# Kernel tuning notes

Measured on AMD Instinct MI355X. Metric: run time of the kernel, lower is better.

## Reference

```python
import jax, jax.numpy as jnp
import numpy as np

N = 100000      # nodes
E = 1600000     # edges (before self-loops)
DIM = 128       # input feature dim
H = 5           # attention heads
C = 10          # per-head output channels
G = 256         # graphs in batch
NEG_SLOPE = 0.2 # PyG GATConv default


def setup_inputs() -> dict:
    key = jax.random.key(0)
    ks = jax.random.split(key, 8)
    x = jax.random.normal(ks[0], (N, DIM), jnp.float32)
    edge_index = jax.random.randint(ks[1], (2, E), 0, N, dtype=jnp.int64)
    batch = jnp.sort(jax.random.randint(ks[2], (N,), 0, G, dtype=jnp.int64))
    W = jax.random.normal(ks[3], (DIM, H * C), jnp.float32) * 0.05
    att_src = jax.random.normal(ks[4], (H, C), jnp.float32) * 0.1
    att_dst = jax.random.normal(ks[5], (H, C), jnp.float32) * 0.1
    bias = jnp.zeros((H * C,), jnp.float32)
    lin_w = jax.random.normal(ks[6], (H * C, 1), jnp.float32) * 0.1
    lin_b = jnp.zeros((1,), jnp.float32)
    return {"x": x, "W": W, "att_src": att_src, "att_dst": att_dst,
            "bias": bias, "lin_w": lin_w, "lin_b": lin_b,
            "edge_index": edge_index, "batch": batch}


def reference(x, W, att_src, att_dst, bias, lin_w, lin_b, edge_index, batch):
    n = x.shape[0]
    # PyG GATConv adds self-loops by default
    loop = jnp.arange(n, dtype=edge_index.dtype)
    src = jnp.concatenate([edge_index[0], loop])  # message sources j
    dst = jnp.concatenate([edge_index[1], loop])  # message targets i

    xw = (x @ W).reshape(n, H, C)                       # [N,H,C]
    a_src = jnp.einsum('nhc,hc->nh', xw, att_src)       # [N,H]
    a_dst = jnp.einsum('nhc,hc->nh', xw, att_dst)       # [N,H]

    logits = jax.nn.leaky_relu(a_src[src] + a_dst[dst], NEG_SLOPE)  # [Etot,H]
    # segment softmax over incoming edges per target node
    m = jax.ops.segment_max(logits, dst, num_segments=n)
    ex = jnp.exp(logits - m[dst])
    denom = jax.ops.segment_sum(ex, dst, num_segments=n)
    alpha = ex / denom[dst]                              # [Etot,H]

    msg = alpha[:, :, None] * xw[src]                    # [Etot,H,C]
    out = jax.ops.segment_sum(msg, dst, num_segments=n).reshape(n, H * C) + bias
    out = jax.nn.elu(out)                                # [N,H*C]

    # global_mean_pool over graph ids
    gsum = jax.ops.segment_sum(out, batch, num_segments=G)
    cnt = jax.ops.segment_sum(jnp.ones((n,), out.dtype), batch, num_segments=G)
    h = gsum / jnp.maximum(cnt, 1.0)[:, None]            # [G,H*C]

    # dropout p=0.5 is identity at inference (training=False)
    y = jax.nn.sigmoid(h @ lin_w + lin_b)                # [G,1]
    return (h, y)
```

## Files before the change

### kernel.cpp

```cpp
#include <hip/hip_runtime.h>
#include <hip/hip_bf16.h>
#include <hip/hip_fp8.h>
#include <math.h>

#define DIM 128
#define H 5
#define C 10
#define HC 50
#define NG 256
#define NEG_SLOPE 0.2f
#define UNR 16
#define WP 136
#define LOG2E 1.4426950408889634f

#define BSH 6
#define NB 1563
#define SB_CAP 1344
#define B1_BLOCKS 391
#define B1_CHUNK 4096

#define BKN2 32
#define ROWS_LDS2 (BKN2 * 64)

typedef short short8 __attribute__((ext_vector_type(8)));
typedef float floatx4 __attribute__((ext_vector_type(4)));
typedef float floatx2 __attribute__((ext_vector_type(2)));

__device__ inline short f2bf(float f) {
  __hip_bfloat16 h = __float2bfloat16(f);
  return *reinterpret_cast<short*>(&h);
}
#if __has_builtin(__builtin_amdgcn_cvt_f32_fp8)
__device__ inline float fp8tof(int b) { return __builtin_amdgcn_cvt_f32_fp8(b, 0); }
#else
__device__ inline float fp8tof(int b) {
  __hip_fp8_e4m3 v;
  v.__x = (__hip_fp8_storage_t)b;
  return (float)v;
}
#endif
#if __has_builtin(__builtin_amdgcn_cvt_pk_f32_fp8)
__device__ inline floatx2 fp8pk2(int us) {
  return __builtin_amdgcn_cvt_pk_f32_fp8(us, false);
}
#else
__device__ inline floatx2 fp8pk2(int us) {
  floatx2 r;
  r.x = fp8tof(us & 0xff);
  r.y = fp8tof((us >> 8) & 0xff);
  return r;
}
#endif
#if __has_builtin(__builtin_amdgcn_exp2f)
__device__ inline float fexp2(float x) { return __builtin_amdgcn_exp2f(x); }
#else
__device__ inline float fexp2(float x) { return exp2f(x); }
#endif
__device__ inline unsigned char ftofp8(float f) {
  __hip_fp8_e4m3 v(f);
  return v.__x;
}

__global__ __launch_bounds__(256) void k_prep(
    const float* __restrict__ W, const float* __restrict__ att_src,
    const float* __restrict__ att_dst, short* __restrict__ swt_g,
    int* __restrict__ gcur, unsigned char* __restrict__ recb, int n) {
  int t = threadIdx.x;
  for (int i = t; i < NB; i += 256) gcur[i] = 0;
  if (t < 64) recb[((size_t)n << 6) + t] = (t < HC) ? 0x00 : 0xFE;
  for (int idx = t; idx < HC * 128; idx += 256) {
    int j = idx >> 7, k = idx & 127;
    swt_g[idx] = f2bf(W[k * HC + j]);
  }
  if (t < 128) {
    float sv[H] = {0.f, 0.f, 0.f, 0.f, 0.f};
    float dv[H] = {0.f, 0.f, 0.f, 0.f, 0.f};
#pragma unroll
    for (int c = 0; c < HC; ++c) {
      float w = W[t * HC + c];
      sv[c / C] += w * att_src[c];
      dv[c / C] += w * att_dst[c];
    }
#pragma unroll
    for (int h = 0; h < H; ++h) {
      swt_g[(HC + h) * 128 + t] = f2bf(sv[h] * LOG2E);
      swt_g[(55 + h) * 128 + t] = f2bf(dv[h] * LOG2E);
    }
  } else {
    int k = t - 128;
    for (int j = 60; j < 64; ++j) swt_g[j * 128 + k] = 0;
  }
}

__global__ __launch_bounds__(256) void k_split(
    const int* __restrict__ src, const int* __restrict__ dst,
    int* __restrict__ gcur, int* __restrict__ seg, int E_) {
  __shared__ int hist[NB], curs[NB], baser[NB];
  int tid = threadIdx.x;
  for (int i = tid; i < NB; i += 256) hist[i] = 0;
  __syncthreads();
  int e0 = blockIdx.x * B1_CHUNK;
  for (int k = 0; k < B1_CHUNK; k += 256) {
    int e = e0 + k + tid;
    if (e < E_) atomicAdd(&hist[((unsigned)dst[e]) >> BSH], 1);
  }
  __syncthreads();
  for (int i = tid; i < NB; i += 256) {
    baser[i] = hist[i] ? atomicAdd(&gcur[i], hist[i]) : 0;
    curs[i] = 0;
  }
  __syncthreads();
  for (int k = 0; k < B1_CHUNK; k += 256) {
    int e = e0 + k + tid;
    if (e < E_) {
      int d = dst[e];
      int s = ((unsigned)d) >> BSH;
      int pos = baser[s] + atomicAdd(&curs[s], 1);
      if (pos < SB_CAP) seg[(size_t)s * SB_CAP + pos] = (src[e] << 6) | (d & 63);
    }
  }
}

__global__ __launch_bounds__(256) void k_mfma(
    const float* __restrict__ x, const short* __restrict__ swt_g,
    unsigned char* __restrict__ recb, __hip_bfloat16* __restrict__ adst, int n) {
  __shared__ short swt[64 * WP];
  for (int idx = threadIdx.x; idx < 1024; idx += 256) {
    int row = idx >> 4;
    *(short8*)&swt[row * WP + (idx & 15) * 8] = *(const short8*)(swt_g + idx * 8);
  }
  __syncthreads();
  int wv = threadIdx.x >> 6, lane = threadIdx.x & 63;
  int tiles = (n + 15) >> 4;
  int tile = blockIdx.x * 4 + wv;
  if (tile >= tiles) return;
  int r = lane & 15, q = lane >> 4;
  int row = tile * 16 + r;
  const float* xr = x + (size_t)min(row, n - 1) * DIM + q * 8;
  floatx4 acc[4];
#pragma unroll
  for (int nt = 0; nt < 4; ++nt) acc[nt] = (floatx4){0.f, 0.f, 0.f, 0.f};
#pragma unroll
  for (int ks = 0; ks < 4; ++ks) {
    float4 a0 = *(const float4*)(xr + ks * 32);
    float4 a1 = *(const float4*)(xr + ks * 32 + 4);
    short8 af;
    af[0] = f2bf(a0.x); af[1] = f2bf(a0.y); af[2] = f2bf(a0.z); af[3] = f2bf(a0.w);
    af[4] = f2bf(a1.x); af[5] = f2bf(a1.y); af[6] = f2bf(a1.z); af[7] = f2bf(a1.w);
    const short* wb = &swt[r * WP + q * 8 + ks * 32];
    short8 b0 = *(const short8*)(wb);
    short8 b1 = *(const short8*)(wb + 16 * WP);
    short8 b2 = *(const short8*)(wb + 32 * WP);
    short8 b3 = *(const short8*)(wb + 48 * WP);
    acc[0] = __builtin_amdgcn_mfma_f32_16x16x32_bf16(af, b0, acc[0], 0, 0, 0);
    acc[1] = __builtin_amdgcn_mfma_f32_16x16x32_bf16(af, b1, acc[1], 0, 0, 0);
    acc[2] = __builtin_amdgcn_mfma_f32_16x16x32_bf16(af, b2, acc[2], 0, 0, 0);
    acc[3] = __builtin_amdgcn_mfma_f32_16x16x32_bf16(af, b3, acc[3], 0, 0, 0);
  }
#pragma unroll
  for (int reg = 0; reg < 4; ++reg) {
    int nrow = tile * 16 + q * 4 + reg;
    if (nrow >= n) continue;
    size_t base = (size_t)nrow << 6;
#pragma unroll
    for (int nt = 0; nt < 4; ++nt) {
      int col = nt * 16 + r;
      float v = acc[nt][reg];
      if (col < 50) {
        recb[base + col] = ftofp8(v);
      } else if (col < 55) {
        unsigned char bv = ftofp8(v);
        *(unsigned short*)(recb + base + 50 + 2 * (col - 50)) =
            (unsigned short)(bv | (bv << 8));
      } else if (col < 60) {
        adst[(size_t)nrow * H + (col - 55)] = __float2bfloat16(v);
      }
    }
  }
}

__global__ __launch_bounds__(256) void k_bin_gat(
    const int* __restrict__ seg, const int* __restrict__ gcur,
    const unsigned char* __restrict__ recb, const __hip_bfloat16* __restrict__ adst,
    const float* __restrict__ bias, float* __restrict__ out_node, int n) {
  __shared__ int rows[ROWS_LDS2];
  int tid = threadIdx.x;
  int blk = blockIdx.x;
  int b = blk >> 1;
  int half32 = blk & 1;
  int lo = (b << BSH) + (half32 << 5);
  int hi = min(lo + BKN2, n);
  for (int k = tid; k < ROWS_LDS2; k += 256) rows[k] = n;
  __syncthreads();
  int cnt = min(gcur[b], SB_CAP);
  for (int k = tid; k < cnt; k += 256) {
    int e = seg[(size_t)b * SB_CAP + k];
    int dl = e & 63;
    if ((dl >> 5) == half32) {
      int s = ((unsigned)e) >> 6;
      int base = (dl & 31) << 6;
      int off = s & 63;
      int old = atomicExch(&rows[base + off], s);
      int probes = 0;
      while (old != n && probes < 128) {
        off = (off + 1) & 63;
        old = atomicExch(&rows[base + off], old);
        ++probes;
      }
    }
  }
  __syncthreads();

  int w = tid >> 6, lane = tid & 63;
  int nn = hi - lo;
  int pairsN = (nn + 1) >> 1;
  int hl = lane & 31;
  int hf = lane >> 5;
  bool chl = hl < 25;
  int h = hl / 5;
  int bpidx = ((hf << 5) + 25 + h) << 2;
  unsigned rowoff = (unsigned)(hl << 1);

  for (int pr = w; pr < pairsN; pr += 4) {
    int i0l = pr * 2;
    int i1l = min(i0l + 1, nn - 1);
    int i0 = lo + i0l, i1 = lo + i1l;
    int iown = hf ? i1 : i0;
    float adi = 0.f;
    if (chl) adi = __bfloat162float(adst[(size_t)iown * H + h]);

    int jraw0 = rows[(i0l << 6) | lane];
    int jraw1 = rows[(i1l << 6) | lane];
    bool v0 = (unsigned)jraw0 < (unsigned)n;
    unsigned long long mk0 = __ballot(v0);
    int deg0 = __popcll(mk0);
    int bel0 = __popcll(mk0 & ((1ull << lane) - 1ull));
    int jc0 = __builtin_amdgcn_ds_permute((v0 ? bel0 : (deg0 + lane - bel0)) << 2,
                                          v0 ? jraw0 : n);
    bool v1 = (unsigned)jraw1 < (unsigned)n;
    unsigned long long mk1 = __ballot(v1);
    int deg1 = __popcll(mk1);
    int bel1 = __popcll(mk1 & ((1ull << lane) - 1ull));
    int jc1 = __builtin_amdgcn_ds_permute((v1 ? bel1 : (deg1 + lane - bel1)) << 2,
                                          v1 ? jraw1 : n);
    int mx = max(deg0, deg1);

    float dpA, dpB = 0.f, a0A, a0B = 0.f, a1A, a1B = 0.f;
    {
      int us = *(const unsigned short*)(recb + (((size_t)(unsigned)iown << 6) | rowoff));
      int asv = __builtin_amdgcn_ds_bpermute(bpidx, us);
      float asi = fp8tof(asv);
      float z = asi + adi;
      z = fmaxf(z, NEG_SLOPE * z);
      float pw = fexp2(z);
      floatx2 f = fp8pk2(us);
      dpA = pw;
      a0A = pw * f.x;
      a1A = pw * f.y;
    }
    for (int s0 = 0; s0 < mx; s0 += UNR) {
      int us[UNR];
#pragma unroll
      for (int u = 0; u < UNR; ++u) {
        int j0 = __builtin_amdgcn_readlane(jc0, s0 + u);
        int j1 = __builtin_amdgcn_readlane(jc1, s0 + u);
        unsigned j = hf ? (unsigned)j1 : (unsigned)j0;
        us[u] = *(const unsigned short*)(recb + (((size_t)j << 6) | rowoff));
      }
#pragma unroll
      for (int u = 0; u < UNR; ++u) {
        int asv = __builtin_amdgcn_ds_bpermute(bpidx, us[u]);
        float asi = fp8tof(asv);
        float z = asi + adi;
        z = fmaxf(z, NEG_SLOPE * z);
        float pw = fexp2(z);
        floatx2 f = fp8pk2(us[u]);
        if (u & 1) {
          dpB += pw;
          a0B = fmaf(pw, f.x, a0B);
          a1B = fmaf(pw, f.y, a1B);
        } else {
          dpA += pw;
          a0A = fmaf(pw, f.x, a0A);
          a1A = fmaf(pw, f.y, a1A);
        }
      }
    }
    if (chl) {
      float dp = dpA + dpB;
      float a0 = a0A + a0B, a1 = a1A + a1B;
      int c0 = hl * 2;
      float o0 = a0 / dp + bias[c0];
      o0 = o0 > 0.f ? o0 : __expf(o0) - 1.f;
      float o1 = a1 / dp + bias[c0 + 1];
      o1 = o1 > 0.f ? o1 : __expf(o1) - 1.f;
      float2 st;
      st.x = o0;
      st.y = o1;
      *(float2*)(out_node + (size_t)iown * HC + c0) = st;
    }
  }
}

__global__ __launch_bounds__(1024) void k_pool(
    const float* __restrict__ out_node, const int* __restrict__ batch,
    const float* __restrict__ lin_w, const float* __restrict__ lin_b,
    float* __restrict__ out, int n) {
  __shared__ int sb[2];
  __shared__ float sacc[16][HC];
  int g = blockIdx.x;
  int t = threadIdx.x;
  if (t < 2) {
    int target = g + t, lo = 0, hi = n;
    while (lo < hi) {
      int mid = (lo + hi) >> 1;
      if (batch[mid] < target) lo = mid + 1; else hi = mid;
    }
    sb[t] = lo;
  }
  __syncthreads();
  int s = sb[0], e = sb[1];
  int w = t >> 6, lane = t & 63;
  float a = 0.f;
  if (lane < HC)
    for (int i = s + w; i < e; i += 16) a += out_node[(size_t)i * HC + lane];
  if (lane < HC) sacc[w][lane] = a;
  __syncthreads();
  if (t < HC) {
    float r0 = 0.f, r1 = 0.f, r2 = 0.f, r3 = 0.f;
#pragma unroll
    for (int k = 0; k < 4; ++k) {
      r0 += sacc[k][t];
      r1 += sacc[4 + k][t];
      r2 += sacc[8 + k][t];
      r3 += sacc[12 + k][t];
    }
    float hv = ((r0 + r1) + (r2 + r3)) / fmaxf((float)(e - s), 1.f);
    out[g * HC + t] = hv;
    sacc[0][t] = hv * lin_w[t];
  }
  __syncthreads();
  if (t == 0) {
    float p = 0.f;
    for (int c = 0; c < HC; ++c) p += sacc[0][c];
    out[NG * HC + g] = 1.f / (1.f + __expf(-(p + lin_b[0])));
  }
}

extern "C" void kernel_launch(void* const* d_in, const int* in_sizes, int n_in,
                              void* d_out, int out_size, void* d_ws, size_t ws_size,
                              hipStream_t stream) {
  const float* x       = (const float*)d_in[0];
  const float* W       = (const float*)d_in[1];
  const float* att_src = (const float*)d_in[2];
  const float* att_dst = (const float*)d_in[3];
  const float* bias    = (const float*)d_in[4];
  const float* lin_w   = (const float*)d_in[5];
  const float* lin_b   = (const float*)d_in[6];
  const int*   eidx    = (const int*)d_in[7];
  const int*   batch   = (const int*)d_in[8];

  int n  = in_sizes[0] / DIM;
  int E_ = in_sizes[7] / 2;
  const int* srcp = eidx;
  const int* dstp = eidx + E_;

  char* p = (char*)d_ws;
  float* out_node = (float*)p; p += (size_t)n * HC * sizeof(float);
  unsigned char* recb = (unsigned char*)p; p += (size_t)(n + 1) * 64;
  __hip_bfloat16* adst = (__hip_bfloat16*)p; p += (size_t)n * H * sizeof(__hip_bfloat16);
  p = (char*)(((uintptr_t)p + 255) & ~(uintptr_t)255);
  short* swt_g = (short*)p; p += 64 * 128 * sizeof(short);
  p = (char*)(((uintptr_t)p + 255) & ~(uintptr_t)255);
  int* gcur = (int*)p; p += NB * sizeof(int);
  p = (char*)(((uintptr_t)p + 255) & ~(uintptr_t)255);
  int* seg = (int*)p; p += (size_t)NB * SB_CAP * sizeof(int);

  float* out = (float*)d_out;

  int tiles = (n + 15) / 16;
  int mfma_blocks = (tiles + 3) / 4;
  int nbk2 = (n + BKN2 - 1) / BKN2;

  k_prep<<<1, 256, 0, stream>>>(W, att_src, att_dst, swt_g, gcur, recb, n);
  k_split<<<B1_BLOCKS, 256, 0, stream>>>(srcp, dstp, gcur, seg, E_);
  k_mfma<<<mfma_blocks, 256, 0, stream>>>(x, swt_g, recb, adst, n);
  k_bin_gat<<<nbk2, 256, 0, stream>>>(seg, gcur, recb, adst, bias, out_node, n);
  k_pool<<<NG, 1024, 0, stream>>>(out_node, batch, lin_w, lin_b, out, n);
}
```

Before: 221.4 us.

## Merge prep into split, cache dst in registers, LDS neighbor lists in GAT

Moves the weight-prep work into an extra block of the edge-split kernel and uses a tiny zeroing kernel for the bucket counters. The split kernel now keeps the dst indices in registers so the second pass does not reload them. The GAT aggregation compacts neighbor indices into a per-wave LDS buffer instead of using ds_permute and readlane, and reads them in int2 pairs with the unroll reduced to 8. The fp8 conversion now uses the packed hardware convert builtin. Together these aim to cut launch overhead, global reloads and scalar readlane cost, at the price of extra LDS traffic and less memory-level parallelism per iteration.

```diff
diff --git a/kernel.cpp b/kernel.cpp
--- a/kernel.cpp
+++ b/kernel.cpp
@@ -9,7 +9,7 @@
 #define HC 50
 #define NG 256
 #define NEG_SLOPE 0.2f
-#define UNR 16
+#define UNR 8
 #define WP 136
 #define LOG2E 1.4426950408889634f
 
@@ -56,53 +56,71 @@
 #else
 __device__ inline float fexp2(float x) { return exp2f(x); }
 #endif
+#if __has_builtin(__builtin_amdgcn_cvt_pk_fp8_f32)
+__device__ inline unsigned ftofp8pk(float a, float b) {
+  return (unsigned)__builtin_amdgcn_cvt_pk_fp8_f32(a, b, 0, false);
+}
+__device__ inline unsigned char ftofp8(float f) {
+  return (unsigned char)(ftofp8pk(f, f) & 0xff);
+}
+#else
 __device__ inline unsigned char ftofp8(float f) {
   __hip_fp8_e4m3 v(f);
   return v.__x;
 }
-
-__global__ __launch_bounds__(256) void k_prep(
+__device__ inline unsigned ftofp8pk(float a, float b) {
+  return (unsigned)ftofp8(a) | ((unsigned)ftofp8(b) << 8);
+}
+#endif
+
+__global__ void k_zero(int* __restrict__ g) {
+  int t = blockIdx.x * blockDim.x + threadIdx.x;
+  if (t < NB) g[t] = 0;
+}
+
+__global__ __launch_bounds__(256) void k_split(
+    const int* __restrict__ src, const int* __restrict__ dst,
+    int* __restrict__ gcur, int* __restrict__ seg,
     const float* __restrict__ W, const float* __restrict__ att_src,
     const float* __restrict__ att_dst, short* __restrict__ swt_g,
-    int* __restrict__ gcur, unsigned char* __restrict__ recb, int n) {
-  int t = threadIdx.x;
-  for (int i = t; i < NB; i += 256) gcur[i] = 0;
-  if (t < 64) recb[((size_t)n << 6) + t] = (t < HC) ? 0x00 : 0xFE;
-  for (int idx = t; idx < HC * 128; idx += 256) {
-    int j = idx >> 7, k = idx & 127;
-    swt_g[idx] = f2bf(W[k * HC + j]);
-  }
-  if (t < 128) {
-    float sv[H] = {0.f, 0.f, 0.f, 0.f, 0.f};
-    float dv[H] = {0.f, 0.f, 0.f, 0.f, 0.f};
-#pragma unroll
-    for (int c = 0; c < HC; ++c) {
-      float w = W[t * HC + c];
-      sv[c / C] += w * att_src[c];
-      dv[c / C] += w * att_dst[c];
-    }
-#pragma unroll
-    for (int h = 0; h < H; ++h) {
-      swt_g[(HC + h) * 128 + t] = f2bf(sv[h] * LOG2E);
-      swt_g[(55 + h) * 128 + t] = f2bf(dv[h] * LOG2E);
-    }
-  } else {
-    int k = t - 128;
-    for (int j = 60; j < 64; ++j) swt_g[j * 128 + k] = 0;
-  }
-}
-
-__global__ __launch_bounds__(256) void k_split(
-    const int* __restrict__ src, const int* __restrict__ dst,
-    int* __restrict__ gcur, int* __restrict__ seg, int E_) {
+    unsigned char* __restrict__ recb, int E_, int n) {
   __shared__ int hist[NB], curs[NB], baser[NB];
   int tid = threadIdx.x;
+  if (blockIdx.x == B1_BLOCKS) {
+    if (tid < 64) recb[((size_t)n << 6) + tid] = (tid < HC) ? 0x00 : 0xFE;
+    for (int idx = tid; idx < HC * 128; idx += 256) {
+      int j = idx >> 7, k = idx & 127;
+      swt_g[idx] = f2bf(W[k * HC + j]);
+    }
+    if (tid < 128) {
+      float sv[H] = {0.f, 0.f, 0.f, 0.f, 0.f};
+      float dv[H] = {0.f, 0.f, 0.f, 0.f, 0.f};
+#pragma unroll
+      for (int c = 0; c < HC; ++c) {
+        float w = W[tid * HC + c];
+        sv[c / C] += w * att_src[c];
+        dv[c / C] += w * att_dst[c];
+      }
+#pragma unroll
+      for (int h = 0; h < H; ++h) {
+        swt_g[(HC + h) * 128 + tid] = f2bf(sv[h] * LOG2E);
+        swt_g[(55 + h) * 128 + tid] = f2bf(dv[h] * LOG2E);
+      }
+    } else {
+      int k = tid - 128;
+      for (int j = 60; j < 64; ++j) swt_g[j * 128 + k] = 0;
+    }
+    return;
+  }
   for (int i = tid; i < NB; i += 256) hist[i] = 0;
   __syncthreads();
   int e0 = blockIdx.x * B1_CHUNK;
-  for (int k = 0; k < B1_CHUNK; k += 256) {
-    int e = e0 + k + tid;
-    if (e < E_) atomicAdd(&hist[((unsigned)dst[e]) >> BSH], 1);
+  int dreg[16];
+#pragma unroll
+  for (int k = 0; k < 16; ++k) {
+    int e = e0 + (k << 8) + tid;
+    dreg[k] = (e < E_) ? dst[e] : -1;
+    if (dreg[k] >= 0) atomicAdd(&hist[((unsigned)dreg[k]) >> BSH], 1);
   }
   __syncthreads();
   for (int i = tid; i < NB; i += 256) {
@@ -110,13 +128,14 @@
     curs[i] = 0;
   }
   __syncthreads();
-  for (int k = 0; k < B1_CHUNK; k += 256) {
-    int e = e0 + k + tid;
-    if (e < E_) {
-      int d = dst[e];
+#pragma unroll
+  for (int k = 0; k < 16; ++k) {
+    if (dreg[k] >= 0) {
+      int d = dreg[k];
       int s = ((unsigned)d) >> BSH;
       int pos = baser[s] + atomicAdd(&curs[s], 1);
-      if (pos < SB_CAP) seg[(size_t)s * SB_CAP + pos] = (src[e] << 6) | (d & 63);
+      if (pos < SB_CAP)
+        seg[(size_t)s * SB_CAP + pos] = (src[e0 + (k << 8) + tid] << 6) | (d & 63);
     }
   }
 }
@@ -169,9 +188,8 @@
       if (col < 50) {
         recb[base + col] = ftofp8(v);
       } else if (col < 55) {
-        unsigned char bv = ftofp8(v);
         *(unsigned short*)(recb + base + 50 + 2 * (col - 50)) =
-            (unsigned short)(bv | (bv << 8));
+            (unsigned short)(ftofp8pk(v, v) & 0xffff);
       } else if (col < 60) {
         adst[(size_t)nrow * H + (col - 55)] = __float2bfloat16(v);
       }
@@ -184,6 +202,7 @@
     const unsigned char* __restrict__ recb, const __hip_bfloat16* __restrict__ adst,
     const float* __restrict__ bias, float* __restrict__ out_node, int n) {
   __shared__ int rows[ROWS_LDS2];
+  __shared__ __align__(16) int wbuf[4][128];
   int tid = threadIdx.x;
   int blk = blockIdx.x;
   int b = blk >> 1;
@@ -212,6 +231,7 @@
   __syncthreads();
 
   int w = tid >> 6, lane = tid & 63;
+  int* wb = wbuf[w];
   int nn = hi - lo;
   int pairsN = (nn + 1) >> 1;
   int hl = lane & 31;
@@ -220,6 +240,7 @@
   int h = hl / 5;
   int bpidx = ((hf << 5) + 25 + h) << 2;
   unsigned rowoff = (unsigned)(hl << 1);
+  int rbase = hf << 6;
 
   for (int pr = w; pr < pairsN; pr += 4) {
     int i0l = pr * 2;
@@ -231,18 +252,17 @@
 
     int jraw0 = rows[(i0l << 6) | lane];
     int jraw1 = rows[(i1l << 6) | lane];
+    ((int2*)wb)[lane] = make_int2(n, n);
     bool v0 = (unsigned)jraw0 < (unsigned)n;
     unsigned long long mk0 = __ballot(v0);
     int deg0 = __popcll(mk0);
     int bel0 = __popcll(mk0 & ((1ull << lane) - 1ull));
-    int jc0 = __builtin_amdgcn_ds_permute((v0 ? bel0 : (deg0 + lane - bel0)) << 2,
-                                          v0 ? jraw0 : n);
+    if (v0) wb[bel0] = jraw0;
     bool v1 = (unsigned)jraw1 < (unsigned)n;
     unsigned long long mk1 = __ballot(v1);
     int deg1 = __popcll(mk1);
     int bel1 = __popcll(mk1 & ((1ull << lane) - 1ull));
-    int jc1 = __builtin_amdgcn_ds_permute((v1 ? bel1 : (deg1 + lane - bel1)) << 2,
-                                          v1 ? jraw1 : n);
+    if (v1) wb[64 + bel1] = jraw1;
     int mx = max(deg0, deg1);
 
     float dpA, dpB = 0.f, a0A, a0B = 0.f, a1A, a1B = 0.f;
@@ -259,22 +279,20 @@
       a1A = pw * f.y;
     }
     for (int s0 = 0; s0 < mx; s0 += UNR) {
-      int us[UNR];
+      int2 jp[UNR / 2];
+#pragma unroll
+      for (int up = 0; up < UNR / 2; ++up)
+        jp[up] = *(const int2*)&wb[rbase + s0 + up * 2];
 #pragma unroll
       for (int u = 0; u < UNR; ++u) {
-        int j0 = __builtin_amdgcn_readlane(jc0, s0 + u);
-        int j1 = __builtin_amdgcn_readlane(jc1, s0 + u);
-        unsigned j = hf ? (unsigned)j1 : (unsigned)j0;
-        us[u] = *(const unsigned short*)(recb + (((size_t)j << 6) | rowoff));
-      }
-#pragma unroll
-      for (int u = 0; u < UNR; ++u) {
-        int asv = __builtin_amdgcn_ds_bpermute(bpidx, us[u]);
+        unsigned j = (unsigned)((u & 1) ? jp[u >> 1].y : jp[u >> 1].x);
+        int us = *(const unsigned short*)(recb + (((size_t)j << 6) | rowoff));
+        int asv = __builtin_amdgcn_ds_bpermute(bpidx, us);
         float asi = fp8tof(asv);
         float z = asi + adi;
         z = fmaxf(z, NEG_SLOPE * z);
         float pw = fexp2(z);
-        floatx2 f = fp8pk2(us[u]);
+        floatx2 f = fp8pk2(us);
         if (u & 1) {
           dpB += pw;
           a0B = fmaf(pw, f.x, a0B);
@@ -382,8 +400,9 @@
   int mfma_blocks = (tiles + 3) / 4;
   int nbk2 = (n + BKN2 - 1) / BKN2;
 
-  k_prep<<<1, 256, 0, stream>>>(W, att_src, att_dst, swt_g, gcur, recb, n);
-  k_split<<<B1_BLOCKS, 256, 0, stream>>>(srcp, dstp, gcur, seg, E_);
+  k_zero<<<2, 1024, 0, stream>>>(gcur);
+  k_split<<<B1_BLOCKS + 1, 256, 0, stream>>>(
+      srcp, dstp, gcur, seg, W, att_src, att_dst, swt_g, recb, E_, n);
   k_mfma<<<mfma_blocks, 256, 0, stream>>>(x, swt_g, recb, adst, n);
   k_bin_gat<<<nbk2, 256, 0, stream>>>(seg, gcur, recb, adst, bias, out_node, n);
   k_pool<<<NG, 1024, 0, stream>>>(out_node, batch, lin_w, lin_b, out, n);
```

Result: faster. 199.0 us (-10.1%).
